# Optimization experiments

Measured on AMD Instinct MI355X. Metric: run time of the kernel, lower is better.

## Reference

```python
import jax, jax.numpy as jnp
import numpy as np

N_NODES = 100000
N_EDGES = 640000
D = 128
N_LAYERS = 4
N_GRAPHS = 512


def setup_inputs() -> dict:
    key = jax.random.key(0)
    ks = jax.random.split(key, 12)
    x = jax.random.normal(ks[0], (N_NODES, D), dtype=jnp.float32)
    edge_index = jax.random.randint(ks[1], (2, N_EDGES), 0, N_NODES, dtype=jnp.int64)
    batch = jnp.sort(jax.random.randint(ks[2], (N_NODES,), 0, N_GRAPHS, dtype=jnp.int64))
    s = 1.0 / np.sqrt(D)
    convW = jax.random.uniform(ks[3], (N_LAYERS, D, D), jnp.float32, -s, s)
    convB = jax.random.uniform(ks[4], (N_LAYERS, D), jnp.float32, -s, s)
    W1 = jax.random.uniform(ks[5], (D, D), jnp.float32, -s, s)
    b1 = jax.random.uniform(ks[6], (D,), jnp.float32, -s, s)
    W2 = jax.random.uniform(ks[7], (D, D), jnp.float32, -s, s)
    b2 = jax.random.uniform(ks[8], (D,), jnp.float32, -s, s)
    W3 = jax.random.uniform(ks[9], (D, 1), jnp.float32, -s, s)
    b3 = jax.random.uniform(ks[10], (1,), jnp.float32, -s, s)
    return {"x": x, "edge_index": edge_index, "batch": batch,
            "convW": convW, "convB": convB,
            "W1": W1, "b1": b1, "W2": W2, "b2": b2, "W3": W3, "b3": b3}


def reference(x, edge_index, batch, convW, convB, W1, b1, W2, b2, W3, b3):
    N = x.shape[0]
    # GCNConv default: add self-loops, symmetric deg^-1/2 normalization
    loops = jnp.arange(N, dtype=edge_index.dtype)
    src = jnp.concatenate([edge_index[0], loops])  # [E+N]
    dst = jnp.concatenate([edge_index[1], loops])
    deg = jax.ops.segment_sum(jnp.ones_like(dst, dtype=x.dtype), dst, num_segments=N)
    dinv = jnp.where(deg > 0, jax.lax.rsqrt(deg), 0.0)
    norm = (dinv[src] * dinv[dst])[:, None]  # [E+N, 1]
    h = x
    for i in range(N_LAYERS):
        hw = h @ convW[i]                                   # [N, D]
        msg = hw[src] * norm                                # gather + scale [E+N, D]
        agg = jax.ops.segment_sum(msg, dst, num_segments=N)  # scatter-add [N, D]
        h = jax.nn.relu(agg + convB[i])
    pooled = jax.ops.segment_sum(h, batch, num_segments=N_GRAPHS)  # [G, D]
    z = jax.nn.relu(pooled @ W1 + b1)
    z = jax.nn.relu(z @ W2 + b2)
    return jax.nn.sigmoid(z @ W3 + b3)  # [G, 1]
```

## Files before the change

kernel.cpp:

```cpp
#include <hip/hip_runtime.h>
#include <math.h>

#define D 128
#define LSTRIDE 136

typedef _Float16 half8 __attribute__((ext_vector_type(8)));
typedef _Float16 half4v __attribute__((ext_vector_type(4)));
typedef float f32x4 __attribute__((ext_vector_type(4)));


__global__ __launch_bounds__(256) void k_bhist(const int* __restrict__ ei, int E,
                                               int edgeBlocks, int NBUK,
                                               int* __restrict__ bukCnt,
                                               const float* __restrict__ convW,
                                               _Float16* __restrict__ Wf) {
    if ((int)blockIdx.x < edgeBlocks) {
        __shared__ int lh[512];
        const int t = threadIdx.x;
        for (int i = t; i < NBUK; i += 256) lh[i] = 0;
        __syncthreads();
        const int base = blockIdx.x * 4096;
#pragma unroll
        for (int k = 0; k < 4; k++) {
            const int e0 = base + k * 1024 + t * 4;
            if (e0 + 3 < E) {
                int4 d4 = *(const int4*)(ei + E + e0);
                atomicAdd(&lh[d4.x >> 8], 1);
                atomicAdd(&lh[d4.y >> 8], 1);
                atomicAdd(&lh[d4.z >> 8], 1);
                atomicAdd(&lh[d4.w >> 8], 1);
            } else {
                for (int e = e0; e < E && e < e0 + 4; e++)
                    atomicAdd(&lh[ei[E + e] >> 8], 1);
            }
        }
        __syncthreads();
        for (int i = t; i < NBUK; i += 256)
            if (lh[i]) atomicAdd(&bukCnt[i], lh[i]);
    } else {
        const int bid = blockIdx.x - edgeBlocks;
        const int l = bid >> 3;
        const int slot = (bid & 7) * 256 + threadIdx.x;
        const float* W = convW + (size_t)l * D * D;
        const int p = slot >> 6, ln = slot & 63;
        const int s = p >> 3, c = p & 7;
        const int kbase = s * 32 + ((ln >> 4) << 3);
        const int n = (c << 4) + (ln & 15);
        half8 hv;
#pragma unroll
        for (int j = 0; j < 8; j++) hv[j] = (_Float16)W[(size_t)(kbase + j) * D + n];
        *(half8*)(Wf + (size_t)l * D * D + (size_t)slot * 8) = hv;
    }
}


__global__ __launch_bounds__(512) void k_bscan(const int* __restrict__ bukCnt,
                                               int* __restrict__ bukPtr,
                                               int* __restrict__ bukCur, int NBUK) {
    __shared__ int sh[512];
    const int t = threadIdx.x;
    sh[t] = (t < NBUK) ? bukCnt[t] : 0;
    __syncthreads();
    for (int off = 1; off < 512; off <<= 1) {
        int v = (t >= off) ? sh[t - off] : 0;
        __syncthreads();
        sh[t] += v;
        __syncthreads();
    }
    if (t < NBUK) {
        int excl = (t == 0) ? 0 : sh[t - 1];
        bukPtr[t] = excl;
        bukCur[t] = excl;
    }
    if (t == NBUK) bukPtr[t] = sh[NBUK - 1];
    else if (NBUK < 512 && t == 511 && NBUK == 512) {}
}


__global__ __launch_bounds__(256) void k_bscat(const int* __restrict__ ei, int E,
                                               int NBUK, int* __restrict__ bukCur,
                                               int2* __restrict__ ebuk) {
    __shared__ int lcnt[512];
    __shared__ int lbase[512];
    const int t = threadIdx.x;
    for (int i = t; i < NBUK; i += 256) lcnt[i] = 0;
    __syncthreads();
    const int base = blockIdx.x * 4096;
    int es[16], ed[16], lr[16];
#pragma unroll
    for (int k = 0; k < 4; k++) {
        const int e0 = base + k * 1024 + t * 4;
        if (e0 + 3 < E) {
            int4 s4 = *(const int4*)(ei + e0);
            int4 d4 = *(const int4*)(ei + E + e0);
            es[k * 4 + 0] = s4.x; ed[k * 4 + 0] = d4.x;
            es[k * 4 + 1] = s4.y; ed[k * 4 + 1] = d4.y;
            es[k * 4 + 2] = s4.z; ed[k * 4 + 2] = d4.z;
            es[k * 4 + 3] = s4.w; ed[k * 4 + 3] = d4.w;
        } else {
#pragma unroll
            for (int j = 0; j < 4; j++) {
                const int e = e0 + j;
                if (e < E) { es[k * 4 + j] = ei[e]; ed[k * 4 + j] = ei[E + e]; }
                else ed[k * 4 + j] = -1;
            }
        }
    }
#pragma unroll
    for (int i = 0; i < 16; i++)
        if (ed[i] >= 0) lr[i] = atomicAdd(&lcnt[ed[i] >> 8], 1);
    __syncthreads();
    for (int i = t; i < NBUK; i += 256)
        lbase[i] = lcnt[i] ? atomicAdd(&bukCur[i], lcnt[i]) : 0;
    __syncthreads();
#pragma unroll
    for (int i = 0; i < 16; i++) {
        if (ed[i] >= 0) {
            int2 e2; e2.x = es[i]; e2.y = ed[i];
            ebuk[lbase[ed[i] >> 8] + lr[i]] = e2;
        }
    }
}


__global__ __launch_bounds__(256) void k_bcount(const int2* __restrict__ ebuk,
                                                const int* __restrict__ bukPtr,
                                                int* __restrict__ counts, int N) {
    __shared__ int cnt[256];
    const int b = blockIdx.x, t = threadIdx.x;
    cnt[t] = 0;
    __syncthreads();
    const int beg = bukPtr[b], end = bukPtr[b + 1];
    for (int i = beg + t; i < end; i += 256) {
        int2 e = ebuk[i];
        atomicAdd(&cnt[e.y & 255], 1);
    }
    __syncthreads();
    const int node = b * 256 + t;
    if (node < N) counts[node] = cnt[t];
}

__global__ __launch_bounds__(256) void k_scan1(const int* __restrict__ counts,
                                               int* __restrict__ rowptrP,
                                               int* __restrict__ bsums,
                                               float* __restrict__ dinv,
                                               int* __restrict__ degHist, int N) {
    __shared__ int sh[256];
    __shared__ int lh[64];
    const int t = threadIdx.x;
    const int base = blockIdx.x * 1024 + t * 4;
    int c[4], pj[4];
#pragma unroll
    for (int j = 0; j < 4; j++) {
        c[j] = (base + j < N) ? counts[base + j] : 0;
        pj[j] = (c[j] + 3) & ~3;
    }
#pragma unroll
    for (int j = 0; j < 4; j++)
        if (base + j < N) dinv[base + j] = rsqrtf((float)(c[j] + 1));

    if (t < 64) lh[t] = 0;
    __syncthreads();
#pragma unroll
    for (int j = 0; j < 4; j++)
        if (base + j < N) atomicAdd(&lh[c[j] < 63 ? c[j] : 63], 1);
    __syncthreads();
    if (t < 64 && lh[t]) atomicAdd(&degHist[t], lh[t]);

    int tsum = pj[0] + pj[1] + pj[2] + pj[3];
    sh[t] = tsum;
    __syncthreads();
    for (int off = 1; off < 256; off <<= 1) {
        int v = (t >= off) ? sh[t - off] : 0;
        __syncthreads();
        sh[t] += v;
        __syncthreads();
    }
    int run = (t == 0) ? 0 : sh[t - 1];
    if (t == 255) bsums[blockIdx.x] = sh[255];
#pragma unroll
    for (int j = 0; j < 4; j++) {
        if (base + j <= N) rowptrP[base + j] = run;
        run += pj[j];
    }
}


__global__ __launch_bounds__(256) void k_fat2(int* __restrict__ rowptrP,
                                              const int* __restrict__ counts,
                                              const int* __restrict__ bsums,
                                              int NB, int N, int scanBlocks,
                                              const int* __restrict__ degHist,
                                              int* __restrict__ degCur,
                                              int* __restrict__ perm,
                                              int* __restrict__ rankOf) {
    if ((int)blockIdx.x < scanBlocks) {
        __shared__ int pre[128];
        const int t = threadIdx.x;
        if (t < 128) pre[t] = (t < NB) ? bsums[t] : 0;
        __syncthreads();
        for (int off = 1; off < 128; off <<= 1) {
            int v = (t >= off && t < 128) ? pre[t - off] : 0;
            __syncthreads();
            if (t < 128) pre[t] += v;
            __syncthreads();
        }
        int i = blockIdx.x * blockDim.x + t;
        if (i <= N) {
            int b = i >> 10;
            int add = (b == 0) ? 0 : pre[b - 1];
            rowptrP[i] += add;
        }
    } else {
        __shared__ int lbase[64], lh[64], gb[64];
        const int t = threadIdx.x;
        const int i = ((int)blockIdx.x - scanBlocks) * blockDim.x + t;
        if (t < 64) lh[t] = 0;
        __syncthreads();
        int deg = 0, lrank = 0;
        const bool v = i < N;
        if (v) {
            int c = counts[i];
            deg = c < 63 ? c : 63;
            lrank = atomicAdd(&lh[deg], 1);
        }
        __syncthreads();
        if (t < 64) gb[t] = lh[t] ? atomicAdd(&degCur[t], lh[t]) : 0;
        if (t == 0) {
            int run = 0;
            for (int d = 63; d >= 0; d--) { lbase[d] = run; run += degHist[d]; }
        }
        __syncthreads();
        if (v) {
            int r = 1 + lbase[deg] + gb[deg] + lrank;
            perm[r] = i;
            rankOf[i] = r;
        }
    }
}


__global__ void k_bfill(const int2* __restrict__ ebuk, const int* __restrict__ bukPtr,
                        const int* __restrict__ rowptrP, int* __restrict__ srcs,
                        const int* __restrict__ rankOf, int NBUK, int N, int NS,
                        const int* __restrict__ perm,
                        const float* __restrict__ dinv,
                        int* __restrict__ rbegR, int* __restrict__ rpenR,
                        float* __restrict__ dinvR, int* __restrict__ sentIdx,
                        const float* __restrict__ x,
                        _Float16* __restrict__ gA, _Float16* __restrict__ gB) {
    const int b = blockIdx.x;
    if (b < NBUK) {
        __shared__ int cur[256];
        const int t = threadIdx.x;
        const int node = b * 256 + t;
        cur[t] = (node < N) ? rowptrP[node] : 0;
        __syncthreads();
        const int beg = bukPtr[b], end = bukPtr[b + 1];
        for (int i = beg + t; i < end; i += 256) {
            int2 e = ebuk[i];
            int p = atomicAdd(&cur[e.y & 255], 1);
            srcs[p] = rankOf[e.x];
        }
    } else {
        __shared__ int pS[16];
        __shared__ float dS[16];
        const int base = (b - NBUK) * 16;
        const int t = threadIdx.x;
        if (t == 0 && base == 0) {
            int4 sv; sv.x = sv.y = sv.z = sv.w = 0; *(int4*)sentIdx = sv;
        }
        if (t < 16) {
            const int r = base + t;
            int p = -1; float dv = 0.f;
            if (r >= 1 && r <= N) {
                p = perm[r];
                rbegR[r] = rowptrP[p];
                rpenR[r] = rowptrP[p + 1];
                dv = dinv[p];
                dinvR[r] = dv;
            } else if (r < NS) {
                rbegR[r] = 0; rpenR[r] = 0; dinvR[r] = 0.f;
            }
            pS[t] = p; dS[t] = dv;
        }
        __syncthreads();
        const int rr = base + (t >> 4);
        if (rr >= NS) return;
        const int j = t & 15;
        const int p = pS[t >> 4];
        if (p >= 0) {
            const float s = dS[t >> 4];
            const float4 v0 = *(const float4*)(x + (size_t)p * D + j * 8);
            const float4 v1 = *(const float4*)(x + (size_t)p * D + j * 8 + 4);
            half8 h;
            h[0] = (_Float16)(v0.x * s); h[1] = (_Float16)(v0.y * s);
            h[2] = (_Float16)(v0.z * s); h[3] = (_Float16)(v0.w * s);
            h[4] = (_Float16)(v1.x * s); h[5] = (_Float16)(v1.y * s);
            h[6] = (_Float16)(v1.z * s); h[7] = (_Float16)(v1.w * s);
            *(half8*)(gA + (size_t)rr * D + j * 8) = h;
        } else {
            half8 z;
#pragma unroll
            for (int j2 = 0; j2 < 8; j2++) z[j2] = (_Float16)0.f;
            *(half8*)(gA + (size_t)rr * D + j * 8) = z;
            *(half8*)(gB + (size_t)rr * D + j * 8) = z;
        }
    }
}


__global__ __launch_bounds__(256, 8) void k_layer(
        const _Float16* __restrict__ gin,
        const int* __restrict__ rbegR, const int* __restrict__ rpenR,
        const int* __restrict__ srcs,
        const int* __restrict__ sentIdx,
        const float* __restrict__ dinvR,
        const int* __restrict__ perm,
        const _Float16* __restrict__ Wf,
        const float* __restrict__ bias,
        _Float16* __restrict__ gout, int N, int last) {
    __shared__ _Float16 S[32 * LSTRIDE];

    const int tid  = threadIdx.x;
    const int w    = tid >> 6;
    const int lane = tid & 63;
    const int q    = lane >> 4;
    const int l16  = lane & 15;
    const int sb   = blockIdx.x * 32;
    const int cb   = l16 * 8;
    const int slot0 = sb + w * 8 + q * 2;

    int bg[2], nc[2];
    int mx = 0;
#pragma unroll
    for (int it = 0; it < 2; it++) {
        bg[it] = rbegR[slot0 + it];
        nc[it] = (rpenR[slot0 + it] - bg[it]) >> 2;
        mx = nc[it] > mx ? nc[it] : mx;
    }

    float a[2][8];
#pragma unroll
    for (int it = 0; it < 2; it++) {
        half8 sv = *(const half8*)(gin + (size_t)(slot0 + it) * D + cb);
#pragma unroll
        for (int j = 0; j < 8; j++) a[it][j] = (float)sv[j];
    }

    int4 cur[2];
#pragma unroll
    for (int it = 0; it < 2; it++) {
        const int* ip = (0 < nc[it]) ? (srcs + bg[it]) : sentIdx;
        cur[it] = *(const int4*)ip;
    }
    for (int ch = 0; ch < mx; ch++) {
        int4 nxt[2];
#pragma unroll
        for (int it = 0; it < 2; it++) {
            const int* ip = (ch + 1 < nc[it]) ? (srcs + bg[it] + (ch + 1) * 4) : sentIdx;
            nxt[it] = *(const int4*)ip;
        }
#pragma unroll
        for (int it = 0; it < 2; it++) {
            half8 v0 = *(const half8*)(gin + (size_t)cur[it].x * D + cb);
            half8 v1 = *(const half8*)(gin + (size_t)cur[it].y * D + cb);
            half8 v2 = *(const half8*)(gin + (size_t)cur[it].z * D + cb);
            half8 v3 = *(const half8*)(gin + (size_t)cur[it].w * D + cb);
#pragma unroll
            for (int j = 0; j < 8; j++)
                a[it][j] += ((float)v0[j] + (float)v1[j]) + ((float)v2[j] + (float)v3[j]);
        }
#pragma unroll
        for (int it = 0; it < 2; it++) cur[it] = nxt[it];
    }

#pragma unroll
    for (int it = 0; it < 2; it++) {
        const float sc = dinvR[slot0 + it];
        const int nl = w * 8 + q * 2 + it;
        half8 o;
#pragma unroll
        for (int j = 0; j < 8; j++) o[j] = (_Float16)(a[it][j] * sc);
        *(half8*)(&S[nl * LSTRIDE + cb]) = o;
    }

    __syncthreads();

    f32x4 acc[4];
#pragma unroll
    for (int c2 = 0; c2 < 4; c2++) acc[c2] = (f32x4){0.f, 0.f, 0.f, 0.f};

    const int tile = w >> 1;
    const int ccb  = (w & 1) * 4;
    const int nl2  = tile * 16 + l16;
#pragma unroll
    for (int s = 0; s < 4; s++) {
        half8 bf = *(const half8*)(&S[nl2 * LSTRIDE + s * 32 + q * 8]);
#pragma unroll
        for (int c2 = 0; c2 < 4; c2++) {
            half8 wh = *(const half8*)(Wf + (size_t)((s * 8 + ccb + c2) * 64 + lane) * 8);
            acc[c2] = __builtin_amdgcn_mfma_f32_16x16x32_f16(wh, bf, acc[c2], 0, 0, 0);
        }
    }

    const int slot2 = sb + nl2;
    if (!last) {
        const float scale = dinvR[slot2];
        _Float16* rp = gout + (size_t)slot2 * D + q * 4;
#pragma unroll
        for (int c2 = 0; c2 < 4; c2++) {
            const int cc = ccb + c2;
            const float4 bc = *(const float4*)(bias + cc * 16 + q * 4);
            half4v o;
            o[0] = (_Float16)(fmaxf(acc[c2][0] + bc.x, 0.f) * scale);
            o[1] = (_Float16)(fmaxf(acc[c2][1] + bc.y, 0.f) * scale);
            o[2] = (_Float16)(fmaxf(acc[c2][2] + bc.z, 0.f) * scale);
            o[3] = (_Float16)(fmaxf(acc[c2][3] + bc.w, 0.f) * scale);
            *(half4v*)(rp + cc * 16) = o;
        }
    } else if (slot2 >= 1 && slot2 <= N) {
        const int node2 = perm[slot2];
        _Float16* rp = gout + (size_t)node2 * D + q * 4;
#pragma unroll
        for (int c2 = 0; c2 < 4; c2++) {
            const int cc = ccb + c2;
            const float4 bc = *(const float4*)(bias + cc * 16 + q * 4);
            half4v o;
            o[0] = (_Float16)fmaxf(acc[c2][0] + bc.x, 0.f);
            o[1] = (_Float16)fmaxf(acc[c2][1] + bc.y, 0.f);
            o[2] = (_Float16)fmaxf(acc[c2][2] + bc.z, 0.f);
            o[3] = (_Float16)fmaxf(acc[c2][3] + bc.w, 0.f);
            *(half4v*)(rp + cc * 16) = o;
        }
    }
}


__global__ __launch_bounds__(256) void k_poolhead(
        const _Float16* __restrict__ h, const int* __restrict__ batch,
        const float* __restrict__ W1, const float* __restrict__ b1,
        const float* __restrict__ W2, const float* __restrict__ b2,
        const float* __restrict__ W3, const float* __restrict__ b3,
        float* __restrict__ out, int N) {
    __shared__ int sb[2];
    __shared__ float part[16][D];
    __shared__ float pool[D];
    __shared__ float z[D];
    __shared__ float red[D];
    __shared__ float pr[2][D];

    const int g = blockIdx.x;
    const int t = threadIdx.x;

    if (t < 2) {
        int target = g + t;
        int lo = 0, hi = N;
        while (lo < hi) {
            int mid = (lo + hi) >> 1;
            if (batch[mid] < target) lo = mid + 1; else hi = mid;
        }
        sb[t] = lo;
    }
    __syncthreads();
    const int rs = sb[0], re = sb[1];

    const int w = t >> 6;
    const int lane = t & 63;
    const int rw = w * 4 + (lane >> 4);
    const int c8 = (lane & 15) * 8;

    float ax[8];
#pragma unroll
    for (int j = 0; j < 8; j++) ax[j] = 0.f;
    for (int r = rs + rw; r < re; r += 16) {
        half8 vv = *(const half8*)(h + (size_t)r * D + c8);
#pragma unroll
        for (int j = 0; j < 8; j++) ax[j] += (float)vv[j];
    }
#pragma unroll
    for (int j = 0; j < 8; j++) part[rw][c8 + j] = ax[j];
    __syncthreads();

    if (t < D) {
        float s = 0.f;
#pragma unroll
        for (int gg = 0; gg < 16; gg++) s += part[gg][t];
        pool[t] = s;
    }
    __syncthreads();

    {
        const int hf = t >> 7, tt = t & 127;
        const int k0 = hf * 64;
        float s = 0.f;
        for (int k = k0; k < k0 + 64; k++) s = fmaf(pool[k], W1[(size_t)k * D + tt], s);
        pr[hf][tt] = s;
    }
    __syncthreads();
    if (t < D) z[t] = fmaxf(pr[0][t] + pr[1][t] + b1[t], 0.f);
    __syncthreads();

    {
        const int hf = t >> 7, tt = t & 127;
        const int k0 = hf * 64;
        float s = 0.f;
        for (int k = k0; k < k0 + 64; k++) s = fmaf(z[k], W2[(size_t)k * D + tt], s);
        pr[hf][tt] = s;
    }
    __syncthreads();
    if (t < D) red[t] = fmaxf(pr[0][t] + pr[1][t] + b2[t], 0.f) * W3[t];
    __syncthreads();
    for (int off = 64; off >= 1; off >>= 1) {
        if (t < off) red[t] += red[t + off];
        __syncthreads();
    }
    if (t == 0) out[g] = 1.f / (1.f + expf(-(red[0] + b3[0])));
}


extern "C" void kernel_launch(void* const* d_in, const int* in_sizes, int n_in,
                              void* d_out, int out_size, void* d_ws, size_t ws_size,
                              hipStream_t stream) {
    const float* x     = (const float*)d_in[0];
    const int*   ei    = (const int*)d_in[1];
    const int*   batch = (const int*)d_in[2];
    const float* convW = (const float*)d_in[3];
    const float* convB = (const float*)d_in[4];
    const float* W1 = (const float*)d_in[5];
    const float* b1 = (const float*)d_in[6];
    const float* W2 = (const float*)d_in[7];
    const float* b2 = (const float*)d_in[8];
    const float* W3 = (const float*)d_in[9];
    const float* b3 = (const float*)d_in[10];
    float* out = (float*)d_out;

    const int N = in_sizes[0] / D;
    const int E = in_sizes[1] / 2;
    const int G = out_size;
    const int NB = (N + 1023) / 1024;
    const int NS = ((N + 1 + 63) / 64) * 64;
    const int NBUK = (N + 255) / 256;

    char* w = (char*)d_ws;
    size_t off = 0;
    auto alloc = [&](size_t bytes) -> char* {
        char* p = w + off;
        off += (bytes + 255) & ~(size_t)255;
        return p;
    };
    float*     dinv   = (float*)alloc((size_t)N * 4);
    _Float16*  gA     = (_Float16*)alloc((size_t)NS * D * 2);
    _Float16*  gB     = (_Float16*)alloc((size_t)NS * D * 2);
    _Float16*  Wf     = (_Float16*)alloc((size_t)4 * D * D * 2);
    int*       counts = (int*)alloc((size_t)N * 4);
    int*       misc   = (int*)alloc((size_t)(512 + 64 + 64) * 4);
    int*       bukCnt = misc;
    int*       degHist= misc + 512;
    int*       degCur = misc + 576;
    int*       bukPtr = (int*)alloc((size_t)(NBUK + 1) * 4);
    int*       bukCur = (int*)alloc((size_t)NBUK * 4);
    int2*      ebuk   = (int2*)alloc((size_t)E * 8);
    int*       rowptrP= (int*)alloc((size_t)(N + 1) * 4);
    int*       srcs   = (int*)alloc((size_t)(E + 3 * N) * 4);
    int*       bsums  = (int*)alloc((size_t)NB * 4);
    int*       perm   = (int*)alloc((size_t)(N + 1) * 4);
    int*       rankOf = (int*)alloc((size_t)N * 4);
    int*       rbegR  = (int*)alloc((size_t)NS * 4);
    int*       rpenR  = (int*)alloc((size_t)NS * 4);
    float*     dinvR  = (float*)alloc((size_t)NS * 4);
    int*       sentIdx= (int*)alloc(16);

    hipMemsetAsync(misc, 0, (size_t)(512 + 64 + 64) * 4, stream);
    hipMemsetAsync(srcs, 0, (size_t)(E + 3 * N) * 4, stream);
    const int edgeBlocks = (E + 4095) / 4096;
    k_bhist<<<edgeBlocks + 32, 256, 0, stream>>>(ei, E, edgeBlocks, NBUK, bukCnt,
                                                 convW, Wf);
    k_bscan<<<1, 512, 0, stream>>>(bukCnt, bukPtr, bukCur, NBUK);
    k_bscat<<<edgeBlocks, 256, 0, stream>>>(ei, E, NBUK, bukCur, ebuk);
    k_bcount<<<NBUK, 256, 0, stream>>>(ebuk, bukPtr, counts, N);
    k_scan1<<<NB, 256, 0, stream>>>(counts, rowptrP, bsums, dinv, degHist, N);
    const int scanBlocks = (N + 1 + 255) / 256;
    const int rankBlocks = (N + 255) / 256;
    k_fat2<<<scanBlocks + rankBlocks, 256, 0, stream>>>(rowptrP, counts, bsums, NB, N,
                                                        scanBlocks,
                                                        degHist, degCur, perm, rankOf);
    const int rowBlocks = NS / 16;
    k_bfill<<<NBUK + rowBlocks, 256, 0, stream>>>(
        ebuk, bukPtr, rowptrP, srcs, rankOf, NBUK, N, NS,
        perm, dinv, rbegR, rpenR, dinvR, sentIdx, x, gA, gB);

    const int layer_grid = NS / 32;
    const _Float16* gi = gA;
    _Float16* go = gB;
    for (int l = 0; l < 4; l++) {
        k_layer<<<layer_grid, 256, 0, stream>>>(gi, rbegR, rpenR, srcs, sentIdx,
                                                dinvR, perm,
                                                Wf + (size_t)l * D * D,
                                                convB + (size_t)l * D,
                                                go, N, l == 3);
        const _Float16* tmp = go;
        go = (_Float16*)gi;
        gi = tmp;
    }

    k_poolhead<<<G, 256, 0, stream>>>(gi, batch, W1, b1, W2, b2, W3, b3, out, N);
}
```

Measured before the change: 336.0 us.

## Fold bucket scan into scatter, fuse bucket count into scan1, split bfill work

Removes the single-block k_bscan kernel: each k_bscat block now redundantly computes the exclusive bucket prefix serially in shared memory, and block 0 writes bukPtr. Bucket cursors become relative offsets zeroed by the existing memset. k_bcount is merged into k_scan1, which counts per-node degrees from four buckets directly in shared memory. The x-to-fp16 conversion in k_bfill is reorganised to iterate by source node with coalesced reads and scattered row writes, separated from the rank table fill and the padding-row zeroing. Together these cut two launches and one pass over counts, at the cost of a redundant serial scan in every scatter block.

```diff
diff --git a/kernel.cpp b/kernel.cpp
--- a/kernel.cpp
+++ b/kernel.cpp
@@ -54,37 +54,27 @@
 }
 
 
-__global__ __launch_bounds__(512) void k_bscan(const int* __restrict__ bukCnt,
+__global__ __launch_bounds__(256) void k_bscat(const int* __restrict__ ei, int E,
+                                               int NBUK,
+                                               const int* __restrict__ bukCnt,
                                                int* __restrict__ bukPtr,
-                                               int* __restrict__ bukCur, int NBUK) {
-    __shared__ int sh[512];
-    const int t = threadIdx.x;
-    sh[t] = (t < NBUK) ? bukCnt[t] : 0;
-    __syncthreads();
-    for (int off = 1; off < 512; off <<= 1) {
-        int v = (t >= off) ? sh[t - off] : 0;
-        __syncthreads();
-        sh[t] += v;
-        __syncthreads();
-    }
-    if (t < NBUK) {
-        int excl = (t == 0) ? 0 : sh[t - 1];
-        bukPtr[t] = excl;
-        bukCur[t] = excl;
-    }
-    if (t == NBUK) bukPtr[t] = sh[NBUK - 1];
-    else if (NBUK < 512 && t == 511 && NBUK == 512) {}
-}
-
-
-__global__ __launch_bounds__(256) void k_bscat(const int* __restrict__ ei, int E,
-                                               int NBUK, int* __restrict__ bukCur,
+                                               int* __restrict__ bukCur,
                                                int2* __restrict__ ebuk) {
+    __shared__ int ptrL[512];
     __shared__ int lcnt[512];
     __shared__ int lbase[512];
     const int t = threadIdx.x;
-    for (int i = t; i < NBUK; i += 256) lcnt[i] = 0;
-    __syncthreads();
+    for (int i = t; i < NBUK; i += 256) { ptrL[i] = bukCnt[i]; lcnt[i] = 0; }
+    __syncthreads();
+    if (t == 0) {
+        int run = 0;
+        for (int i = 0; i < NBUK; i++) { int c = ptrL[i]; ptrL[i] = run; run += c; }
+    }
+    __syncthreads();
+    if (blockIdx.x == 0) {
+        for (int i = t; i < NBUK; i += 256) bukPtr[i] = ptrL[i];
+        if (t == 0) bukPtr[NBUK] = ptrL[NBUK - 1] + bukCnt[NBUK - 1];
+    }
     const int base = blockIdx.x * 4096;
     int es[16], ed[16], lr[16];
 #pragma unroll
@@ -111,7 +101,7 @@
         if (ed[i] >= 0) lr[i] = atomicAdd(&lcnt[ed[i] >> 8], 1);
     __syncthreads();
     for (int i = t; i < NBUK; i += 256)
-        lbase[i] = lcnt[i] ? atomicAdd(&bukCur[i], lcnt[i]) : 0;
+        lbase[i] = lcnt[i] ? (ptrL[i] + atomicAdd(&bukCur[i], lcnt[i])) : 0;
     __syncthreads();
 #pragma unroll
     for (int i = 0; i < 16; i++) {
@@ -123,53 +113,52 @@
 }
 
 
-__global__ __launch_bounds__(256) void k_bcount(const int2* __restrict__ ebuk,
-                                                const int* __restrict__ bukPtr,
-                                                int* __restrict__ counts, int N) {
-    __shared__ int cnt[256];
-    const int b = blockIdx.x, t = threadIdx.x;
-    cnt[t] = 0;
-    __syncthreads();
-    const int beg = bukPtr[b], end = bukPtr[b + 1];
-    for (int i = beg + t; i < end; i += 256) {
-        int2 e = ebuk[i];
-        atomicAdd(&cnt[e.y & 255], 1);
-    }
-    __syncthreads();
-    const int node = b * 256 + t;
-    if (node < N) counts[node] = cnt[t];
-}
-
-__global__ __launch_bounds__(256) void k_scan1(const int* __restrict__ counts,
+__global__ __launch_bounds__(256) void k_scan1(const int2* __restrict__ ebuk,
+                                               const int* __restrict__ bukPtr,
+                                               int* __restrict__ counts,
                                                int* __restrict__ rowptrP,
                                                int* __restrict__ bsums,
                                                float* __restrict__ dinv,
-                                               int* __restrict__ degHist, int N) {
+                                               int* __restrict__ degHist,
+                                               int N, int NBUK) {
+    __shared__ int cnt[1024];
     __shared__ int sh[256];
     __shared__ int lh[64];
     const int t = threadIdx.x;
-    const int base = blockIdx.x * 1024 + t * 4;
+    const int base0 = blockIdx.x * 1024;
+#pragma unroll
+    for (int j = 0; j < 4; j++) cnt[j * 256 + t] = 0;
+    if (t < 64) lh[t] = 0;
+    __syncthreads();
+
+    const int bk0 = blockIdx.x * 4;
+    const int bkE = (bk0 + 4 < NBUK) ? bk0 + 4 : NBUK;
+    if (bk0 < NBUK) {
+        const int beg = bukPtr[bk0], end = bukPtr[bkE];
+        for (int i = beg + t; i < end; i += 256)
+            atomicAdd(&cnt[ebuk[i].y - base0], 1);
+    }
+    __syncthreads();
+
+    const int base = base0 + t * 4;
     int c[4], pj[4];
 #pragma unroll
     for (int j = 0; j < 4; j++) {
-        c[j] = (base + j < N) ? counts[base + j] : 0;
+        c[j] = (base + j < N) ? cnt[t * 4 + j] : 0;
         pj[j] = (c[j] + 3) & ~3;
     }
 #pragma unroll
     for (int j = 0; j < 4; j++)
-        if (base + j < N) dinv[base + j] = rsqrtf((float)(c[j] + 1));
-
-    if (t < 64) lh[t] = 0;
-    __syncthreads();
-#pragma unroll
-    for (int j = 0; j < 4; j++)
-        if (base + j < N) atomicAdd(&lh[c[j] < 63 ? c[j] : 63], 1);
-    __syncthreads();
-    if (t < 64 && lh[t]) atomicAdd(&degHist[t], lh[t]);
+        if (base + j < N) {
+            counts[base + j] = c[j];
+            dinv[base + j] = rsqrtf((float)(c[j] + 1));
+            atomicAdd(&lh[c[j] < 63 ? c[j] : 63], 1);
+        }
 
     int tsum = pj[0] + pj[1] + pj[2] + pj[3];
     sh[t] = tsum;
     __syncthreads();
+    if (t < 64 && lh[t]) atomicAdd(&degHist[t], lh[t]);
     for (int off = 1; off < 256; off <<= 1) {
         int v = (t >= off) ? sh[t - off] : 0;
         __syncthreads();
@@ -243,6 +232,7 @@
 __global__ void k_bfill(const int2* __restrict__ ebuk, const int* __restrict__ bukPtr,
                         const int* __restrict__ rowptrP, int* __restrict__ srcs,
                         const int* __restrict__ rankOf, int NBUK, int N, int NS,
+                        int tabBlocks, int cvtBlocks,
                         const int* __restrict__ perm,
                         const float* __restrict__ dinv,
                         int* __restrict__ rbegR, int* __restrict__ rpenR,
@@ -262,50 +252,44 @@
             int p = atomicAdd(&cur[e.y & 255], 1);
             srcs[p] = rankOf[e.x];
         }
-    } else {
-        __shared__ int pS[16];
-        __shared__ float dS[16];
-        const int base = (b - NBUK) * 16;
-        const int t = threadIdx.x;
-        if (t == 0 && base == 0) {
-            int4 sv; sv.x = sv.y = sv.z = sv.w = 0; *(int4*)sentIdx = sv;
-        }
-        if (t < 16) {
-            const int r = base + t;
-            int p = -1; float dv = 0.f;
+    } else if (b < NBUK + tabBlocks) {
+        const int r = (b - NBUK) * 256 + threadIdx.x;
+        if (r == 0) { int4 sv; sv.x = sv.y = sv.z = sv.w = 0; *(int4*)sentIdx = sv; }
+        if (r < NS) {
             if (r >= 1 && r <= N) {
-                p = perm[r];
+                int p = perm[r];
                 rbegR[r] = rowptrP[p];
                 rpenR[r] = rowptrP[p + 1];
-                dv = dinv[p];
-                dinvR[r] = dv;
-            } else if (r < NS) {
+                dinvR[r] = dinv[p];
+            } else {
                 rbegR[r] = 0; rpenR[r] = 0; dinvR[r] = 0.f;
             }
-            pS[t] = p; dS[t] = dv;
-        }
-        __syncthreads();
-        const int rr = base + (t >> 4);
-        if (rr >= NS) return;
-        const int j = t & 15;
-        const int p = pS[t >> 4];
-        if (p >= 0) {
-            const float s = dS[t >> 4];
-            const float4 v0 = *(const float4*)(x + (size_t)p * D + j * 8);
-            const float4 v1 = *(const float4*)(x + (size_t)p * D + j * 8 + 4);
-            half8 h;
-            h[0] = (_Float16)(v0.x * s); h[1] = (_Float16)(v0.y * s);
-            h[2] = (_Float16)(v0.z * s); h[3] = (_Float16)(v0.w * s);
-            h[4] = (_Float16)(v1.x * s); h[5] = (_Float16)(v1.y * s);
-            h[6] = (_Float16)(v1.z * s); h[7] = (_Float16)(v1.w * s);
-            *(half8*)(gA + (size_t)rr * D + j * 8) = h;
-        } else {
-            half8 z;
-#pragma unroll
-            for (int j2 = 0; j2 < 8; j2++) z[j2] = (_Float16)0.f;
-            *(half8*)(gA + (size_t)rr * D + j * 8) = z;
-            *(half8*)(gB + (size_t)rr * D + j * 8) = z;
-        }
+        }
+    } else if (b < NBUK + tabBlocks + cvtBlocks) {
+        const int idx = (b - NBUK - tabBlocks) * 256 + threadIdx.x;
+        if (idx >= N * 16) return;
+        const int node = idx >> 4, j = idx & 15;
+        const int rr = rankOf[node];
+        const float s = dinv[node];
+        const float4 v0 = *(const float4*)(x + (size_t)node * D + j * 8);
+        const float4 v1 = *(const float4*)(x + (size_t)node * D + j * 8 + 4);
+        half8 h;
+        h[0] = (_Float16)(v0.x * s); h[1] = (_Float16)(v0.y * s);
+        h[2] = (_Float16)(v0.z * s); h[3] = (_Float16)(v0.w * s);
+        h[4] = (_Float16)(v1.x * s); h[5] = (_Float16)(v1.y * s);
+        h[6] = (_Float16)(v1.z * s); h[7] = (_Float16)(v1.w * s);
+        *(half8*)(gA + (size_t)rr * D + j * 8) = h;
+    } else {
+        const int idx = (b - NBUK - tabBlocks - cvtBlocks) * 256 + threadIdx.x;
+        const int nd = NS - N;
+        if (idx >= nd * 16) return;
+        const int k = idx >> 4, j = idx & 15;
+        const int r = (k == 0) ? 0 : N + k;
+        half8 z;
+#pragma unroll
+        for (int j2 = 0; j2 < 8; j2++) z[j2] = (_Float16)0.f;
+        *(half8*)(gA + (size_t)r * D + j * 8) = z;
+        *(half8*)(gB + (size_t)r * D + j * 8) = z;
     }
 }
 
@@ -554,12 +538,12 @@
     _Float16*  gB     = (_Float16*)alloc((size_t)NS * D * 2);
     _Float16*  Wf     = (_Float16*)alloc((size_t)4 * D * D * 2);
     int*       counts = (int*)alloc((size_t)N * 4);
-    int*       misc   = (int*)alloc((size_t)(512 + 64 + 64) * 4);
+    int*       misc   = (int*)alloc((size_t)(512 + 512 + 64 + 64) * 4);
     int*       bukCnt = misc;
-    int*       degHist= misc + 512;
-    int*       degCur = misc + 576;
+    int*       bukCur = misc + 512;
+    int*       degHist= misc + 1024;
+    int*       degCur = misc + 1088;
     int*       bukPtr = (int*)alloc((size_t)(NBUK + 1) * 4);
-    int*       bukCur = (int*)alloc((size_t)NBUK * 4);
     int2*      ebuk   = (int2*)alloc((size_t)E * 8);
     int*       rowptrP= (int*)alloc((size_t)(N + 1) * 4);
     int*       srcs   = (int*)alloc((size_t)(E + 3 * N) * 4);
@@ -571,23 +555,24 @@
     float*     dinvR  = (float*)alloc((size_t)NS * 4);
     int*       sentIdx= (int*)alloc(16);
 
-    hipMemsetAsync(misc, 0, (size_t)(512 + 64 + 64) * 4, stream);
+    hipMemsetAsync(misc, 0, (size_t)(512 + 512 + 64 + 64) * 4, stream);
     hipMemsetAsync(srcs, 0, (size_t)(E + 3 * N) * 4, stream);
     const int edgeBlocks = (E + 4095) / 4096;
     k_bhist<<<edgeBlocks + 32, 256, 0, stream>>>(ei, E, edgeBlocks, NBUK, bukCnt,
                                                  convW, Wf);
-    k_bscan<<<1, 512, 0, stream>>>(bukCnt, bukPtr, bukCur, NBUK);
-    k_bscat<<<edgeBlocks, 256, 0, stream>>>(ei, E, NBUK, bukCur, ebuk);
-    k_bcount<<<NBUK, 256, 0, stream>>>(ebuk, bukPtr, counts, N);
-    k_scan1<<<NB, 256, 0, stream>>>(counts, rowptrP, bsums, dinv, degHist, N);
+    k_bscat<<<edgeBlocks, 256, 0, stream>>>(ei, E, NBUK, bukCnt, bukPtr, bukCur, ebuk);
+    k_scan1<<<NB, 256, 0, stream>>>(ebuk, bukPtr, counts, rowptrP, bsums, dinv,
+                                    degHist, N, NBUK);
     const int scanBlocks = (N + 1 + 255) / 256;
     const int rankBlocks = (N + 255) / 256;
     k_fat2<<<scanBlocks + rankBlocks, 256, 0, stream>>>(rowptrP, counts, bsums, NB, N,
                                                         scanBlocks,
                                                         degHist, degCur, perm, rankOf);
-    const int rowBlocks = NS / 16;
-    k_bfill<<<NBUK + rowBlocks, 256, 0, stream>>>(
-        ebuk, bukPtr, rowptrP, srcs, rankOf, NBUK, N, NS,
+    const int tabBlocks  = (NS + 255) / 256;
+    const int cvtBlocks  = (N * 16 + 255) / 256;
+    const int zeroBlocks = ((NS - N) * 16 + 255) / 256;
+    k_bfill<<<NBUK + tabBlocks + cvtBlocks + zeroBlocks, 256, 0, stream>>>(
+        ebuk, bukPtr, rowptrP, srcs, rankOf, NBUK, N, NS, tabBlocks, cvtBlocks,
         perm, dinv, rbegR, rpenR, dinvR, sentIdx, x, gA, gB);
 
     const int layer_grid = NS / 32;
```

Result: no change. 338.4 us (+0.7%).
